# Kernel optimization log

Measured on AMD Instinct MI355X. Metric: run time of the kernel, lower is better.

## Reference

```python
import jax, jax.numpy as jnp
from jax import lax
import numpy as np

# Keras LSTM cell semantics: gate order [i, f, c(candidate), o];
# recurrent_activation = sigmoid, activation = act (relu for all layers except
# the final decoder LSTM which uses tanh). h = o * act(c).

def lstm_layer(x, W, U, b, act, return_sequences):
    # x: [B, T, I], W: [I, 4H], U: [H, 4H], b: [4H]
    B = x.shape[0]
    H = U.shape[0]
    xW = jnp.einsum('bti,ih->bth', x, W) + b  # precompute input projections
    def step(carry, xw_t):
        h, c = carry
        z = xw_t + h @ U                      # [B, 4H]
        i, f, g, o = jnp.split(z, 4, axis=-1)
        i = jax.nn.sigmoid(i)
        f = jax.nn.sigmoid(f)
        g = act(g)
        o = jax.nn.sigmoid(o)
        c = f * c + i * g
        h = o * act(c)
        return (h, c), h
    h0 = jnp.zeros((B, H), x.dtype)
    (hT, _), hs = lax.scan(step, (h0, h0), jnp.swapaxes(xW, 0, 1))
    if return_sequences:
        return jnp.swapaxes(hs, 0, 1)         # [B, T, H]
    return hT                                  # [B, H]

# layer dims: (in, hidden) for enc0, enc1, enc_latent, dec0, dec1, dec_out
LAYER_DIMS = [(256, 512), (512, 256), (256, 64), (64, 256), (256, 512), (512, 256)]

def setup_inputs() -> dict:
    key = jax.random.key(0)
    keys = jax.random.split(key, 1 + 3 * len(LAYER_DIMS))
    inp = {'x': jax.random.normal(keys[0], (64, 256, 256), dtype=jnp.float32)}
    for li, (din, dh) in enumerate(LAYER_DIMS):
        kw, ku, _ = keys[1 + 3 * li], keys[2 + 3 * li], keys[3 + 3 * li]
        sW = 1.0 / np.sqrt(din)
        sU = 1.0 / np.sqrt(dh)
        inp[f'W{li}'] = jax.random.normal(kw, (din, 4 * dh), dtype=jnp.float32) * sW
        inp[f'U{li}'] = jax.random.normal(ku, (dh, 4 * dh), dtype=jnp.float32) * sU
        inp[f'b{li}'] = jnp.zeros((4 * dh,), dtype=jnp.float32)
    return inp

def reference(x, W0, U0, b0, W1, U1, b1, W2, U2, b2, W3, U3, b3, W4, U4, b4, W5, U5, b5):
    relu = jax.nn.relu
    # encoder: relu LSTMs, all return_sequences=True
    h = lstm_layer(x, W0, U0, b0, relu, True)
    h = lstm_layer(h, W1, U1, b1, relu, True)
    h = lstm_layer(h, W2, U2, b2, relu, True)   # latent_dim=64
    # decoder: relu LSTMs then final tanh LSTM with return_sequences=False
    h = lstm_layer(h, W3, U3, b3, relu, True)
    h = lstm_layer(h, W4, U4, b4, relu, True)
    out = lstm_layer(h, W5, U5, b5, jnp.tanh, False)  # [B, input_size]
    return out
```

## Files before the change

### kernel.cpp

```cpp
#include <hip/hip_runtime.h>
#include <stdint.h>

#define AGENT __HIP_MEMORY_SCOPE_AGENT
typedef unsigned long long u64;

__global__ __launch_bounds__(256) void xpose_in(const float* __restrict__ x,
                                                float* __restrict__ xT) {
  const int t = blockIdx.x;
  const int b = threadIdx.x & 63;
  const int w = threadIdx.x >> 6;
  const float* xr = x + ((size_t)b * 256 + t) * 256;
  float* o = xT + (size_t)t * 256 * 64;
  for (int kq = w * 16; kq < w * 16 + 16; ++kq) {
    float4 v = *(const float4*)(xr + kq * 4);
    o[(size_t)(kq * 4 + 0) * 64 + b] = v.x;
    o[(size_t)(kq * 4 + 1) * 64 + b] = v.y;
    o[(size_t)(kq * 4 + 2) * 64 + b] = v.z;
    o[(size_t)(kq * 4 + 3) * 64 + b] = v.w;
  }
}

__global__ __launch_bounds__(256) void pack_wu(const float* __restrict__ W,
                                               const float* __restrict__ U,
                                               float* __restrict__ out,
                                               int DIN, int H) {
  __shared__ float tile[64][65];
  const int KT = DIN + H;
  const int KTq = KT >> 2;
  const int c0 = blockIdx.x * 64;
  const int k0 = blockIdx.y * 64;
  const int tx = threadIdx.x & 63;
  const int ty = threadIdx.x >> 6;
  for (int r = ty; r < 64; r += 4) {
    const int k = k0 + r;
    tile[r][tx] = (k < DIN) ? W[(size_t)k * (4 * H) + c0 + tx]
                            : U[(size_t)(k - DIN) * (4 * H) + c0 + tx];
  }
  __syncthreads();
  for (int r = ty; r < 64; r += 4) {
    const int cg = c0 + r;
    const int g = cg / H;
    const int col = cg - g * H;
    const int wg = col >> 2;
    const int jl = col & 3;
    const int c = (g << 2) | jl;
    const int k = k0 + tx;
    const int q = k >> 2;
    const int j = k & 3;
    out[(((size_t)wg * KTq + q) * 16 + c) * 4 + j] = tile[tx][r];
  }
}

#define SB __builtin_amdgcn_sched_barrier(0)
#define FMA_K4(A_, W_, M_)                                            \
  A_ = fmaf((W_).x, x0_.M_, A_); A_ = fmaf((W_).y, x1_.M_, A_);       \
  A_ = fmaf((W_).z, x2_.M_, A_); A_ = fmaf((W_).w, x3_.M_, A_);
#define FMA_ROW16(W_, O_)      \
  FMA_K4(acc[(O_) + 0], W_, x) \
  FMA_K4(acc[(O_) + 1], W_, y) \
  FMA_K4(acc[(O_) + 2], W_, z) \
  FMA_K4(acc[(O_) + 3], W_, w)

template <int QW>
__device__ __forceinline__ void accum_cb(const float4* __restrict__ src4,
                                         const float4* __restrict__ wl4,
                                         int bq, int cq4, float acc[16]) {
  static_assert(QW % 4 == 0, "grouping assumes 4|QW");
#pragma unroll 1
  for (int g = 0; g < QW; g += 4) {
#pragma unroll
    for (int ql = g; ql < g + 4; ++ql) {
      const float4 x0_ = src4[(size_t)ql * 64 + 0 * 16 + bq];
      const float4 x1_ = src4[(size_t)ql * 64 + 1 * 16 + bq];
      const float4 x2_ = src4[(size_t)ql * 64 + 2 * 16 + bq];
      const float4 x3_ = src4[(size_t)ql * 64 + 3 * 16 + bq];
      const float4 w0_ = wl4[ql * 16 + cq4 + 0];
      const float4 w1_ = wl4[ql * 16 + cq4 + 1];
      const float4 w2_ = wl4[ql * 16 + cq4 + 2];
      const float4 w3_ = wl4[ql * 16 + cq4 + 3];
      FMA_ROW16(w0_, 0)
      FMA_ROW16(w1_, 4)
      FMA_ROW16(w2_, 8)
      FMA_ROW16(w3_, 12)
    }
    SB;
  }
}

template <int NWG>
__device__ __forceinline__ void agg_body(unsigned* __restrict__ flg,
                                         unsigned* __restrict__ ep) {
  const int tid = threadIdx.x;
  if (tid >= 64) return;
  for (int t = 0; t < 256; ++t) {
    unsigned* base = flg + (size_t)t * NWG;
    if (NWG <= 64) {
      if (tid < NWG) {
        while (__hip_atomic_load(base + tid, __ATOMIC_RELAXED, AGENT) == 0u)
          __builtin_amdgcn_s_sleep(1);
      }
    } else {
      while (__hip_atomic_load(base + tid, __ATOMIC_RELAXED, AGENT) == 0u)
        __builtin_amdgcn_s_sleep(1);
      while (__hip_atomic_load(base + 64 + tid, __ATOMIC_RELAXED, AGENT) == 0u)
        __builtin_amdgcn_s_sleep(1);
    }
    asm volatile("s_waitcnt vmcnt(0)" ::: "memory");
    if (tid == 0)
      __hip_atomic_store(ep, (unsigned)(t + 1), __ATOMIC_RELAXED, AGENT);
  }
}

template <int DIN, int H, int NWG, bool FIN, bool XCOH>
__device__ __forceinline__ void layer_body(
    int wg, int tid, const float* __restrict__ xin, float* __restrict__ hseq,
    const float* __restrict__ wP, const float* __restrict__ bias,
    float* __restrict__ dout, unsigned* __restrict__ selfF,
    unsigned* __restrict__ selfE, unsigned* __restrict__ prevE,
    float* __restrict__ wL, float (*sZ)[16][64], float* sH) {
  constexpr int KT = DIN + H;
  constexpr int KTq = KT / 4;
  constexpr int QX = DIN / 16;
  constexpr int QH = H / 16;
  constexpr int T = 256;
  static_assert(QX % 4 == 0 && QH % 4 == 0, "grouping assumes 4|QW");

  const int lane = tid & 63;
  const int wv = tid >> 6;
  const int bq = lane & 15;
  const int cq4 = (lane >> 4) * 4;

  {
    float4* wl = (float4*)wL;
    const float4* wp = (const float4*)wP + (size_t)wg * KTq * 16;
    for (int i = tid; i < KTq * 16; i += 256) wl[i] = wp[i];
  }
  const float4* wl4x = (const float4*)wL + (size_t)wv * QX * 16;
  const float4* wl4h = (const float4*)wL + ((size_t)(DIN / 4) + wv * QH) * 16;

  float bz[4];
#pragma unroll
  for (int g = 0; g < 4; ++g) bz[g] = bias[g * H + wg * 4 + wv];
  float cst = 0.f;
  __syncthreads();

  for (int t = 0; t < T; ++t) {
    float acc[16];
#pragma unroll
    for (int c = 0; c < 16; ++c) acc[c] = 0.f;

    if (!XCOH) {
      accum_cb<QX>((const float4*)(xin + (size_t)t * DIN * 64) +
                       (size_t)wv * QX * 64,
                   wl4x, bq, cq4, acc);
    }
    if (t > 0 && tid == 0) {
      while (__hip_atomic_load(selfE, __ATOMIC_RELAXED, AGENT) < (unsigned)t)
        __builtin_amdgcn_s_sleep(2);
    }
    if (XCOH && tid == 64) {
      while (__hip_atomic_load(prevE, __ATOMIC_RELAXED, AGENT) <
             (unsigned)(t + 1))
        __builtin_amdgcn_s_sleep(2);
    }
    __syncthreads();
    asm volatile("" ::: "memory");

    if (XCOH) {
      accum_cb<QX>((const float4*)(xin + (size_t)t * DIN * 64) +
                       (size_t)wv * QX * 64,
                   wl4x, bq, cq4, acc);
    }
    if (t > 0) {
      accum_cb<QH>((const float4*)(hseq + (size_t)(t - 1) * H * 64) +
                       (size_t)wv * QH * 64,
                   wl4h, bq, cq4, acc);
    }

#pragma unroll
    for (int i = 0; i < 4; ++i) {
      *(float4*)&sZ[wv][cq4 + i][bq * 4] = make_float4(
          acc[i * 4 + 0], acc[i * 4 + 1], acc[i * 4 + 2], acc[i * 4 + 3]);
    }
    __syncthreads();

    float z[4];
#pragma unroll
    for (int g = 0; g < 4; ++g) {
      z[g] = bz[g];
#pragma unroll
      for (int k = 0; k < 4; ++k) z[g] += sZ[k][g * 4 + wv][lane];
    }
    const float ig = 1.f / (1.f + __expf(-z[0]));
    const float fg = 1.f / (1.f + __expf(-z[1]));
    const float gg = FIN ? tanhf(z[2]) : fmaxf(z[2], 0.f);
    const float og = 1.f / (1.f + __expf(-z[3]));
    cst = fg * cst + ig * gg;
    const float ca = FIN ? tanhf(cst) : fmaxf(cst, 0.f);
    const float h = og * ca;
    sH[lane * 4 + wv] = h;
    if (FIN && t == T - 1) dout[(size_t)lane * H + wg * 4 + wv] = h;
    __syncthreads();

    if (wv == 0) {
      float* hw = hseq + (size_t)t * H * 64 + (size_t)(wg * 4) * 64 + lane;
#pragma unroll
      for (int jl = 0; jl < 4; ++jl) {
        __hip_atomic_store(hw + jl * 64, sH[lane * 4 + jl], __ATOMIC_RELAXED,
                           AGENT);
      }
      asm volatile("s_waitcnt vmcnt(0)" ::: "memory");
      if (tid == 0)
        __hip_atomic_store(&selfF[t * NWG + wg], 1u, __ATOMIC_RELAXED, AGENT);
    }
  }
}

__global__ __launch_bounds__(256, 2) void lstm_fused(
    const float* __restrict__ xT, float* __restrict__ h0,
    float* __restrict__ h1, float* __restrict__ h2, float* __restrict__ h3,
    float* __restrict__ h4, float* __restrict__ h5,
    const float* __restrict__ wuT0, const float* __restrict__ wuT1,
    const float* __restrict__ wuT2, const float* __restrict__ wuT3,
    const float* __restrict__ wuT4, const float* __restrict__ wuT5,
    const float* __restrict__ b0, const float* __restrict__ b1,
    const float* __restrict__ b2, const float* __restrict__ b3,
    const float* __restrict__ b4, const float* __restrict__ b5,
    float* __restrict__ dout, unsigned* __restrict__ f0,
    unsigned* __restrict__ f1, unsigned* __restrict__ f2,
    unsigned* __restrict__ f3, unsigned* __restrict__ f4,
    unsigned* __restrict__ f5, unsigned* __restrict__ eps) {
  __shared__ alignas(16) float wLDS[16 * 768];
  __shared__ alignas(16) float sZ[4][16][64];
  __shared__ alignas(16) float sH[256];
  const int b = blockIdx.x;
  const int tid = threadIdx.x;
  if (b < 128) {
    layer_body<256, 512, 128, false, false>(b, tid, xT, h0, wuT0, b0, nullptr,
                                            f0, eps + 0, nullptr, wLDS, sZ, sH);
  } else if (b < 256) {
    layer_body<256, 512, 128, false, true>(b - 128, tid, h3, h4, wuT4, b4,
                                           nullptr, f4, eps + 4, eps + 3, wLDS,
                                           sZ, sH);
  } else if (b < 320) {
    layer_body<512, 256, 64, false, true>(b - 256, tid, h0, h1, wuT1, b1,
                                          nullptr, f1, eps + 1, eps + 0, wLDS,
                                          sZ, sH);
  } else if (b < 384) {
    layer_body<64, 256, 64, false, true>(b - 320, tid, h2, h3, wuT3, b3,
                                         nullptr, f3, eps + 3, eps + 2, wLDS,
                                         sZ, sH);
  } else if (b < 448) {
    layer_body<512, 256, 64, true, true>(b - 384, tid, h4, h5, wuT5, b5, dout,
                                         f5, eps + 5, eps + 4, wLDS, sZ, sH);
  } else if (b < 464) {
    layer_body<256, 64, 16, false, true>(b - 448, tid, h1, h2, wuT2, b2,
                                         nullptr, f2, eps + 2, eps + 1, wLDS,
                                         sZ, sH);
  } else {
    const int l = b - 464;
    if (l == 0) agg_body<128>(f0, eps + 0);
    else if (l == 1) agg_body<64>(f1, eps + 1);
    else if (l == 2) agg_body<16>(f2, eps + 2);
    else if (l == 3) agg_body<64>(f3, eps + 3);
    else if (l == 4) agg_body<128>(f4, eps + 4);
    else agg_body<64>(f5, eps + 5);
  }
}

extern "C" void kernel_launch(void* const* d_in, const int* in_sizes, int n_in,
                              void* d_out, int out_size, void* d_ws,
                              size_t ws_size, hipStream_t stream) {
  (void)in_sizes; (void)n_in; (void)out_size; (void)ws_size;
  const float* x = (const float*)d_in[0];
  const float* W[6];
  const float* U[6];
  const float* B[6];
  for (int l = 0; l < 6; ++l) {
    W[l] = (const float*)d_in[1 + 3 * l];
    U[l] = (const float*)d_in[2 + 3 * l];
    B[l] = (const float*)d_in[3 + 3 * l];
  }
  char* ws = (char*)d_ws;
  unsigned* f0 = (unsigned*)ws;
  unsigned* f1 = f0 + 128 * 256;
  unsigned* f2 = f1 + 64 * 256;
  unsigned* f3 = f2 + 16 * 256;
  unsigned* f4 = f3 + 64 * 256;
  unsigned* f5 = f4 + 128 * 256;
  unsigned* eps = f0 + 464 * 256;
  float* wuT0 = (float*)(ws + (1u << 20));
  float* wuT1 = wuT0 + (size_t)2048 * 768;
  float* wuT2 = wuT1 + (size_t)1024 * 768;
  float* wuT3 = wuT2 + (size_t)256 * 320;
  float* wuT4 = wuT3 + (size_t)1024 * 320;
  float* wuT5 = wuT4 + (size_t)2048 * 768;
  float* xT = (float*)(ws + (22u << 20));
  float* h0 = (float*)(ws + (38u << 20));
  float* h1 = (float*)(ws + (70u << 20));
  float* h2 = (float*)(ws + (86u << 20));
  float* h3 = (float*)(ws + (90u << 20));
  float* h4 = (float*)(ws + (106u << 20));
  float* h5 = (float*)(ws + (138u << 20));

  hipMemsetAsync(f0, 0, (464 * 256 + 8) * sizeof(unsigned), stream);
  xpose_in<<<256, 256, 0, stream>>>(x, xT);
  pack_wu<<<dim3(32, 12), 256, 0, stream>>>(W[0], U[0], wuT0, 256, 512);
  pack_wu<<<dim3(16, 12), 256, 0, stream>>>(W[1], U[1], wuT1, 512, 256);
  pack_wu<<<dim3(4, 5), 256, 0, stream>>>(W[2], U[2], wuT2, 256, 64);
  pack_wu<<<dim3(16, 5), 256, 0, stream>>>(W[3], U[3], wuT3, 64, 256);
  pack_wu<<<dim3(32, 12), 256, 0, stream>>>(W[4], U[4], wuT4, 256, 512);
  pack_wu<<<dim3(16, 12), 256, 0, stream>>>(W[5], U[5], wuT5, 512, 256);

  lstm_fused<<<470, 256, 0, stream>>>(xT, h0, h1, h2, h3, h4, h5, wuT0, wuT1,
                                      wuT2, wuT3, wuT4, wuT5, B[0], B[1], B[2],
                                      B[3], B[4], B[5], (float*)d_out, f0, f1,
                                      f2, f3, f4, f5, eps);
}
```

Baseline: 3.826 ms.

## Retile recurrent GEMV to 8x8 register blocks with 16-way K-slicing and swizzle reduction

Replaces the 4x4-per-thread accumulation with an 8-column x 8-batch register tile per lane, splitting K across 16 slices (4 per wave) instead of 4 wave slices. Partial sums across the 4 K-slices within a wave are reduced with ds_swizzle butterflies before a single lane group writes to shared memory. The goal is higher arithmetic intensity per shared-memory load in the serial per-timestep matmul. In exchange, each thread holds 64 accumulators, which raises register pressure and can lower occupancy, and the 128 swizzle ops add cross-lane work every step.

```diff
diff --git a/kernel.cpp b/kernel.cpp
--- a/kernel.cpp
+++ b/kernel.cpp
@@ -52,38 +52,44 @@
 }
 
 #define SB __builtin_amdgcn_sched_barrier(0)
-#define FMA_K4(A_, W_, M_)                                            \
-  A_ = fmaf((W_).x, x0_.M_, A_); A_ = fmaf((W_).y, x1_.M_, A_);       \
-  A_ = fmaf((W_).z, x2_.M_, A_); A_ = fmaf((W_).w, x3_.M_, A_);
-#define FMA_ROW16(W_, O_)      \
-  FMA_K4(acc[(O_) + 0], W_, x) \
-  FMA_K4(acc[(O_) + 1], W_, y) \
-  FMA_K4(acc[(O_) + 2], W_, z) \
-  FMA_K4(acc[(O_) + 3], W_, w)
-
-template <int QW>
-__device__ __forceinline__ void accum_cb(const float4* __restrict__ src4,
-                                         const float4* __restrict__ wl4,
-                                         int bq, int cq4, float acc[16]) {
-  static_assert(QW % 4 == 0, "grouping assumes 4|QW");
+#define FMA_B8(I_, WS_, XA_, XB_)                                   \
+  acc[(I_) * 8 + 0] = fmaf(WS_, (XA_).x, acc[(I_) * 8 + 0]);        \
+  acc[(I_) * 8 + 1] = fmaf(WS_, (XA_).y, acc[(I_) * 8 + 1]);        \
+  acc[(I_) * 8 + 2] = fmaf(WS_, (XA_).z, acc[(I_) * 8 + 2]);        \
+  acc[(I_) * 8 + 3] = fmaf(WS_, (XA_).w, acc[(I_) * 8 + 3]);        \
+  acc[(I_) * 8 + 4] = fmaf(WS_, (XB_).x, acc[(I_) * 8 + 4]);        \
+  acc[(I_) * 8 + 5] = fmaf(WS_, (XB_).y, acc[(I_) * 8 + 5]);        \
+  acc[(I_) * 8 + 6] = fmaf(WS_, (XB_).z, acc[(I_) * 8 + 6]);        \
+  acc[(I_) * 8 + 7] = fmaf(WS_, (XB_).w, acc[(I_) * 8 + 7]);
+#define FMA_ROW32(I_, WV_)                 \
+  FMA_B8(I_, (WV_).x, x0a_, x0b_)          \
+  FMA_B8(I_, (WV_).y, x1a_, x1b_)          \
+  FMA_B8(I_, (WV_).z, x2a_, x2b_)          \
+  FMA_B8(I_, (WV_).w, x3a_, x3b_)
+
+template <int QL>
+__device__ __forceinline__ void accum88(const float4* __restrict__ sp,
+                                        const float4* __restrict__ wp,
+                                        float acc[64]) {
 #pragma unroll 1
-  for (int g = 0; g < QW; g += 4) {
-#pragma unroll
-    for (int ql = g; ql < g + 4; ++ql) {
-      const float4 x0_ = src4[(size_t)ql * 64 + 0 * 16 + bq];
-      const float4 x1_ = src4[(size_t)ql * 64 + 1 * 16 + bq];
-      const float4 x2_ = src4[(size_t)ql * 64 + 2 * 16 + bq];
-      const float4 x3_ = src4[(size_t)ql * 64 + 3 * 16 + bq];
-      const float4 w0_ = wl4[ql * 16 + cq4 + 0];
-      const float4 w1_ = wl4[ql * 16 + cq4 + 1];
-      const float4 w2_ = wl4[ql * 16 + cq4 + 2];
-      const float4 w3_ = wl4[ql * 16 + cq4 + 3];
-      FMA_ROW16(w0_, 0)
-      FMA_ROW16(w1_, 4)
-      FMA_ROW16(w2_, 8)
-      FMA_ROW16(w3_, 12)
-    }
+  for (int q = 0; q < QL; ++q) {
+    const float4 x0a_ = sp[0],  x0b_ = sp[1];
+    const float4 x1a_ = sp[16], x1b_ = sp[17];
+    const float4 x2a_ = sp[32], x2b_ = sp[33];
+    const float4 x3a_ = sp[48], x3b_ = sp[49];
+    const float4 w0_ = wp[0], w1_ = wp[1], w2_ = wp[2], w3_ = wp[3];
+    const float4 w4_ = wp[4], w5_ = wp[5], w6_ = wp[6], w7_ = wp[7];
+    FMA_ROW32(0, w0_)
+    FMA_ROW32(1, w1_)
+    FMA_ROW32(2, w2_)
+    FMA_ROW32(3, w3_)
+    FMA_ROW32(4, w4_)
+    FMA_ROW32(5, w5_)
+    FMA_ROW32(6, w6_)
+    FMA_ROW32(7, w7_)
     SB;
+    sp += 64;
+    wp += 16;
   }
 }
 
@@ -120,23 +126,24 @@
     float* __restrict__ wL, float (*sZ)[16][64], float* sH) {
   constexpr int KT = DIN + H;
   constexpr int KTq = KT / 4;
-  constexpr int QX = DIN / 16;
-  constexpr int QH = H / 16;
+  constexpr int QLX = DIN / 64;
+  constexpr int QLH = H / 64;
   constexpr int T = 256;
-  static_assert(QX % 4 == 0 && QH % 4 == 0, "grouping assumes 4|QW");
+  static_assert(DIN % 64 == 0 && H % 64 == 0, "16-way K-slicing");
 
   const int lane = tid & 63;
   const int wv = tid >> 6;
-  const int bq = lane & 15;
-  const int cq4 = (lane >> 4) * 4;
+  const int cq = lane >> 5;
+  const int k4 = (lane >> 3) & 3;
+  const int bq = lane & 7;
+  const int slice = wv * 4 + k4;
 
   {
     float4* wl = (float4*)wL;
     const float4* wp = (const float4*)wP + (size_t)wg * KTq * 16;
     for (int i = tid; i < KTq * 16; i += 256) wl[i] = wp[i];
   }
-  const float4* wl4x = (const float4*)wL + (size_t)wv * QX * 16;
-  const float4* wl4h = (const float4*)wL + ((size_t)(DIN / 4) + wv * QH) * 16;
+  const float4* wl4 = (const float4*)wL;
 
   float bz[4];
 #pragma unroll
@@ -145,14 +152,14 @@
   __syncthreads();
 
   for (int t = 0; t < T; ++t) {
-    float acc[16];
-#pragma unroll
-    for (int c = 0; c < 16; ++c) acc[c] = 0.f;
+    float acc[64];
+#pragma unroll
+    for (int c = 0; c < 64; ++c) acc[c] = 0.f;
 
     if (!XCOH) {
-      accum_cb<QX>((const float4*)(xin + (size_t)t * DIN * 64) +
-                       (size_t)wv * QX * 64,
-                   wl4x, bq, cq4, acc);
+      accum88<QLX>((const float4*)(xin + (size_t)t * DIN * 64) +
+                       (size_t)slice * QLX * 64 + bq * 2,
+                   wl4 + (size_t)slice * QLX * 16 + cq * 8, acc);
     }
     if (t > 0 && tid == 0) {
       while (__hip_atomic_load(selfE, __ATOMIC_RELAXED, AGENT) < (unsigned)t)
@@ -167,20 +174,39 @@
     asm volatile("" ::: "memory");
 
     if (XCOH) {
-      accum_cb<QX>((const float4*)(xin + (size_t)t * DIN * 64) +
-                       (size_t)wv * QX * 64,
-                   wl4x, bq, cq4, acc);
+      accum88<QLX>((const float4*)(xin + (size_t)t * DIN * 64) +
+                       (size_t)slice * QLX * 64 + bq * 2,
+                   wl4 + (size_t)slice * QLX * 16 + cq * 8, acc);
     }
     if (t > 0) {
-      accum_cb<QH>((const float4*)(hseq + (size_t)(t - 1) * H * 64) +
-                       (size_t)wv * QH * 64,
-                   wl4h, bq, cq4, acc);
-    }
-
-#pragma unroll
-    for (int i = 0; i < 4; ++i) {
-      *(float4*)&sZ[wv][cq4 + i][bq * 4] = make_float4(
-          acc[i * 4 + 0], acc[i * 4 + 1], acc[i * 4 + 2], acc[i * 4 + 3]);
+      accum88<QLH>((const float4*)(hseq + (size_t)(t - 1) * H * 64) +
+                       (size_t)slice * QLH * 64 + bq * 2,
+                   wl4 + (size_t)(DIN / 4 + slice * QLH) * 16 + cq * 8, acc);
+    }
+
+#pragma unroll
+    for (int r = 0; r < 64; ++r) {
+      const int v = __builtin_amdgcn_ds_swizzle(__float_as_int(acc[r]),
+                                                0x201F);
+      acc[r] += __int_as_float(v);
+    }
+#pragma unroll
+    for (int r = 0; r < 64; ++r) {
+      const int v = __builtin_amdgcn_ds_swizzle(__float_as_int(acc[r]),
+                                                0x401F);
+      acc[r] += __int_as_float(v);
+    }
+
+    if (k4 == 0) {
+#pragma unroll
+      for (int i = 0; i < 8; ++i) {
+#pragma unroll
+        for (int h = 0; h < 2; ++h) {
+          *(float4*)&sZ[wv][cq * 8 + i][bq * 8 + h * 4] =
+              make_float4(acc[i * 8 + h * 4 + 0], acc[i * 8 + h * 4 + 1],
+                          acc[i * 8 + h * 4 + 2], acc[i * 8 + h * 4 + 3]);
+        }
+      }
     }
     __syncthreads();
 
```

Measured after the change: 3.460 ms. 9.6% less time.
